# Performance work log

Hardware: AMD Instinct MI355X
Metric: run time of the kernel (lower is better)

The kernel has to match this reference:

```python
import jax, jax.numpy as jnp
import numpy as np

N = 100000
E = 3200000
D_IN = 128
D_OUT = 128


def setup_inputs() -> dict:
    key = jax.random.key(0)
    k1, k2, k3, k4, k5, k6, k7 = jax.random.split(key, 7)
    stdv = 1.0 / np.sqrt(D_OUT)
    x = jax.random.normal(k1, (N, D_IN), dtype=jnp.float32)
    rows = jax.random.randint(k2, (E,), 0, N, dtype=jnp.int32)
    cols = jax.random.randint(k3, (E,), 0, N, dtype=jnp.int32)
    edge_w = jax.random.uniform(k4, (E,), dtype=jnp.float32)
    W = jax.random.uniform(k5, (D_IN, D_OUT), minval=-stdv, maxval=stdv, dtype=jnp.float32)
    W_skip = jax.random.uniform(k6, (D_IN, D_OUT), minval=-stdv, maxval=stdv, dtype=jnp.float32)
    b = jax.random.uniform(k7, (D_OUT,), minval=-stdv, maxval=stdv, dtype=jnp.float32)
    return {"x": x, "rows": rows, "cols": cols, "edge_w": edge_w,
            "W": W, "W_skip": W_skip, "b": b}


def reference(x, rows, cols, edge_w, W, W_skip, b):
    # support1 = x @ W  [N, D_OUT]
    support1 = jnp.dot(x, W)
    # spmm(norm_adj, support1): out[r] = sum_{(r,c) in E} w_rc * support1[c]
    msgs = support1[cols] * edge_w[:, None]          # [E, D_OUT] gather
    agg = jax.ops.segment_sum(msgs, rows, num_segments=N)  # [N, D_OUT] scatter-add
    # skip connection + bias
    out = agg + jnp.dot(x, W_skip) + b
    return out
```

## Files before the change

kernel.cpp:

```cpp
#include <hip/hip_runtime.h>

#define D 128
#define B_LOG 7
#define ROWS_PB 128
#define MAX_NB 1024
#define GEMM_GRID 784
#define CHUNK_LOG 12

typedef short bf16x8 __attribute__((ext_vector_type(8)));
typedef float f32x4  __attribute__((ext_vector_type(4)));

static __device__ __forceinline__ unsigned short f2bf(float f) {
    unsigned u = __float_as_uint(f);
    u += 0x7FFFu + ((u >> 16) & 1u);
    return (unsigned short)(u >> 16);
}

__global__ __launch_bounds__(256) void wconv_kernel(
    const float* __restrict__ W, const float* __restrict__ Ws,
    short* __restrict__ Wt, int* __restrict__ bhist, int nb)
{
    const int idx = blockIdx.x * 256 + threadIdx.x;
    if (idx < 2 * D * D) {
        const int mat = idx >> 14;
        const int rem = idx & (D * D - 1);
        const int n = rem >> 7, k = rem & (D - 1);
        const float* src = mat ? Ws : W;
        Wt[idx] = (short)f2bf(src[k * D + n]);
    }
    if (idx < nb) bhist[idx] = 0;
}

__global__ __launch_bounds__(256) void bhist_kernel(
    const int* __restrict__ rows, int* __restrict__ bhist, int E, int nb)
{
    __shared__ int h[MAX_NB];
    const int t = threadIdx.x;
    for (int i = t; i < nb; i += 256) h[i] = 0;
    __syncthreads();

    int i = blockIdx.x * 256 + t;
    const int stride = gridDim.x * 256;
    for (; i < E; i += stride) atomicAdd(&h[rows[i] >> B_LOG], 1);
    __syncthreads();

    for (int i2 = t; i2 < nb; i2 += 256) {
        const int c = h[i2];
        if (c) atomicAdd(&bhist[i2], c);
    }
}

__global__ __launch_bounds__(256) void bscan_kernel(
    const int* __restrict__ bhist, int* __restrict__ bptr,
    int* __restrict__ bcur, int nb)
{
    const int t = threadIdx.x;
    const int base_i = t * 4;
    int v[4];
#pragma unroll
    for (int k = 0; k < 4; ++k)
        v[k] = (base_i + k < nb) ? bhist[base_i + k] : 0;
    const int s = v[0] + v[1] + v[2] + v[3];

    const int lane = t & 63, wv = t >> 6;
    int sc = s;
    for (int o = 1; o < 64; o <<= 1) {
        const int u = __shfl_up(sc, o, 64);
        if (lane >= o) sc += u;
    }
    __shared__ int wsum[4];
    if (lane == 63) wsum[wv] = sc;
    __syncthreads();

    int wbase = 0;
    for (int w2 = 0; w2 < wv; ++w2) wbase += wsum[w2];
    int excl = wbase + (sc - s);
#pragma unroll
    for (int k = 0; k < 4; ++k) {
        if (base_i + k < nb) { bptr[base_i + k] = excl; bcur[base_i + k] = excl; }
        excl += v[k];
    }
    if (t == 255) bptr[nb] = wsum[0] + wsum[1] + wsum[2] + wsum[3];
}

__global__ __launch_bounds__(256) void gemm_part_kernel(
    const float* __restrict__ x, const short* __restrict__ Wt,
    const float* __restrict__ b, unsigned short* __restrict__ s1b,
    unsigned short* __restrict__ skipb, int N,
    const int* __restrict__ rows, const int* __restrict__ cols,
    const float* __restrict__ ew, int* __restrict__ bcur,
    int2* __restrict__ se1, int E, int nb)
{
    __shared__ short sx[64 * D];

    const int t = threadIdx.x;

    if (blockIdx.x >= GEMM_GRID) {
        int* h = (int*)sx;
        const int nbl = gridDim.x - GEMM_GRID;
        const int nchunks = (E + (1 << CHUNK_LOG) - 1) >> CHUNK_LOG;

        for (int c = blockIdx.x - GEMM_GRID; c < nchunks; c += nbl) {
            const int ebeg = c << CHUNK_LOG;
            const int eend = min(ebeg + (1 << CHUNK_LOG), E);

            for (int i = t; i < nb; i += 256) h[i] = 0;
            __syncthreads();

            for (int e = ebeg + t; e < eend; e += 256)
                atomicAdd(&h[rows[e] >> B_LOG], 1);
            __syncthreads();

            for (int i = t; i < nb; i += 256) {
                const int cnt = h[i];
                h[i] = cnt ? atomicAdd(&bcur[i], cnt) : 0;
            }
            __syncthreads();

            for (int e = ebeg + t; e < eend; e += 256) {
                const int r    = rows[e];
                const int bkt  = r >> B_LOG;
                const int slot = atomicAdd(&h[bkt], 1);
                se1[slot] = make_int2(((r & (ROWS_PB - 1)) << 20) | cols[e],
                                      __float_as_int(ew[e]));
            }
            __syncthreads();
        }
        return;
    }

    const int lane = t & 63;
    const int w    = t >> 6;

    const int bmat = w >> 1;
    const int bn0  = (w & 1) * 64 + (lane & 15);
    const int bk0  = (lane >> 4) * 8;
    bf16x8 Bf[4][4];
#pragma unroll
    for (int nf = 0; nf < 4; ++nf)
#pragma unroll
        for (int ks = 0; ks < 4; ++ks)
            Bf[nf][ks] = *(const bf16x8*)&Wt[
                ((size_t)bmat * D + bn0 + nf * 16) * D + ks * 32 + bk0];

    float bias[4];
#pragma unroll
    for (int nf = 0; nf < 4; ++nf)
        bias[nf] = (w >= 2) ? b[(w - 2) * 64 + nf * 16 + (lane & 15)] : 0.f;

    const int ntiles = (N + 63) >> 6;
    const int trow = t >> 2;
    const int tk   = (t & 3) * 4;

    for (int rt = blockIdx.x; rt < ntiles; rt += GEMM_GRID) {
        const int r0 = rt << 6;
        __syncthreads();

        const int grow = min(r0 + trow, N - 1);
        const float* xrow = &x[(size_t)grow * D];
#pragma unroll
        for (int i = 0; i < 8; ++i) {
            const int k = tk + i * 16;
            const float4 v = *(const float4*)&xrow[k];
            const unsigned lo = (unsigned)f2bf(v.x) | ((unsigned)f2bf(v.y) << 16);
            const unsigned hi = (unsigned)f2bf(v.z) | ((unsigned)f2bf(v.w) << 16);
            unsigned byte = trow * 256 + k * 2;
            byte ^= (unsigned)((trow & 7) << 4);
            *(uint2*)((char*)sx + byte) = make_uint2(lo, hi);
        }
        __syncthreads();

        f32x4 acc[4][4];
#pragma unroll
        for (int mf = 0; mf < 4; ++mf)
#pragma unroll
            for (int nf = 0; nf < 4; ++nf)
                acc[mf][nf] = (f32x4){0.f, 0.f, 0.f, 0.f};

#pragma unroll
        for (int ks = 0; ks < 4; ++ks) {
            bf16x8 Af[4];
#pragma unroll
            for (int mf = 0; mf < 4; ++mf) {
                const int row = mf * 16 + (lane & 15);
                unsigned byte = row * 256 + (ks * 32 + bk0) * 2;
                byte ^= (unsigned)((row & 7) << 4);
                Af[mf] = *(const bf16x8*)((const char*)sx + byte);
            }
#pragma unroll
            for (int mf = 0; mf < 4; ++mf)
#pragma unroll
                for (int nf = 0; nf < 4; ++nf)
                    acc[mf][nf] = __builtin_amdgcn_mfma_f32_16x16x32_bf16(
                        Af[mf], Bf[nf][ks], acc[mf][nf], 0, 0, 0);
        }

#pragma unroll
        for (int mf = 0; mf < 4; ++mf) {
#pragma unroll
            for (int i = 0; i < 4; ++i) {
                const int row = r0 + mf * 16 + (lane >> 4) * 4 + i;
                if (row < N) {
                    if (w < 2) {
#pragma unroll
                        for (int nf = 0; nf < 4; ++nf) {
                            const int col = w * 64 + nf * 16 + (lane & 15);
                            s1b[(size_t)row * D + col] = f2bf(acc[mf][nf][i]);
                        }
                    } else {
#pragma unroll
                        for (int nf = 0; nf < 4; ++nf) {
                            const int col = (w - 2) * 64 + nf * 16 + (lane & 15);
                            skipb[(size_t)row * D + col] =
                                f2bf(acc[mf][nf][i] + bias[nf]);
                        }
                    }
                }
            }
        }
    }
}

__global__ __launch_bounds__(512) void binsort_kernel(
    const int* __restrict__ bptr, const int2* __restrict__ se1,
    int2* __restrict__ se2, int* __restrict__ rowptr, int N, int E)
{
    __shared__ int cnt[ROWS_PB];
    __shared__ int pos[ROWS_PB];
    const int t  = threadIdx.x;
    const int bk = blockIdx.x;
    const int r0 = bk << B_LOG;
    const int nr = min(ROWS_PB, N - r0);

    const int beg = bptr[bk];
    const int end = bptr[bk + 1];

    if (t < ROWS_PB) cnt[t] = 0;
    __syncthreads();

    for (int e = beg + t; e < end; e += 512)
        atomicAdd(&cnt[se1[e].x >> 20], 1);
    __syncthreads();

    if (t < ROWS_PB) pos[t] = cnt[t];
    __syncthreads();
#pragma unroll
    for (int off = 1; off < ROWS_PB; off <<= 1) {
        int v = (t < ROWS_PB && t >= off) ? pos[t - off] : 0;
        __syncthreads();
        if (t < ROWS_PB) pos[t] += v;
        __syncthreads();
    }
    if (t < ROWS_PB) {
        const int excl = beg + pos[t] - cnt[t];
        cnt[t] = excl;
        if (t < nr) rowptr[r0 + t] = excl;
    }
    if (t == 0 && r0 + nr == N) rowptr[N] = E;
    __syncthreads();

    for (int e = beg + t; e < end; e += 512) {
        const int2 rec = se1[e];
        const int  rl  = rec.x >> 20;
        const int  slot = atomicAdd(&cnt[rl], 1);
        se2[slot] = rec;
    }
}

__global__ __launch_bounds__(256) void spmm_csr_kernel(
    const unsigned short* __restrict__ s1b,
    const unsigned short* __restrict__ skipb,
    const int* __restrict__ rowptr, const int2* __restrict__ se,
    float* __restrict__ out, int N)
{
    const int lane = threadIdx.x & 63;
    const int wave = blockIdx.x * 4 + (threadIdx.x >> 6);
    const int nw   = gridDim.x * 4;
    const int j    = lane * 2;

    const long long* seq = (const long long*)se;

    for (int r = wave; r < N; r += nw) {
        const int beg = rowptr[r];
        const int end = rowptr[r + 1];

        float2 acc = make_float2(0.f, 0.f);
        int e = beg;
        for (; e + 8 <= end; e += 8) {
            long long ed[8];
#pragma unroll
            for (int k = 0; k < 8; ++k) ed[k] = seq[e + k];
            unsigned pk[8];
#pragma unroll
            for (int k = 0; k < 8; ++k)
                pk[k] = *(const unsigned*)&s1b[
                    (size_t)((unsigned)ed[k] & 0xFFFFFu) * D + j];
#pragma unroll
            for (int k = 0; k < 8; ++k) {
                const float w = __int_as_float((int)(ed[k] >> 32));
                acc.x = fmaf(w, __uint_as_float(pk[k] << 16), acc.x);
                acc.y = fmaf(w, __uint_as_float(pk[k] & 0xFFFF0000u), acc.y);
            }
        }
        for (; e < end; ++e) {
            const long long ed = seq[e];
            const unsigned pk = *(const unsigned*)&s1b[
                (size_t)((unsigned)ed & 0xFFFFFu) * D + j];
            const float w = __int_as_float((int)(ed >> 32));
            acc.x = fmaf(w, __uint_as_float(pk << 16), acc.x);
            acc.y = fmaf(w, __uint_as_float(pk & 0xFFFF0000u), acc.y);
        }

        const unsigned sk = *(const unsigned*)&skipb[(size_t)r * D + j];
        float2 o;
        o.x = acc.x + __uint_as_float(sk << 16);
        o.y = acc.y + __uint_as_float(sk & 0xFFFF0000u);
        *(float2*)&out[(size_t)r * D + j] = o;
    }
}

__global__ __launch_bounds__(512) void dual_gemm_fb_kernel(
    const float* __restrict__ x, const float* __restrict__ W,
    const float* __restrict__ Ws, const float* __restrict__ b,
    unsigned short* __restrict__ s1b, float* __restrict__ out, int N)
{
    __shared__ float sW[D * D];
    __shared__ float sWs[D * D];

    const int t = threadIdx.x;
    for (int i = t * 4; i < D * D; i += 512 * 4) {
        *(float4*)&sW[i]  = *(const float4*)&W[i];
        *(float4*)&sWs[i] = *(const float4*)&Ws[i];
    }
    __syncthreads();

    const int lane   = t & 63;
    const int wave   = blockIdx.x * 8 + (t >> 6);
    const int nwaves = gridDim.x * 8;
    const int j      = lane * 2;
    const float2 bb  = *(const float2*)&b[j];

    for (int r0 = wave * 4; r0 < N; r0 += nwaves * 4) {
        float2 xr[4];
#pragma unroll
        for (int r = 0; r < 4; ++r)
            xr[r] = *(const float2*)&x[(size_t)(r0 + r) * D + j];

        float2 a1[4], a2[4];
#pragma unroll
        for (int r = 0; r < 4; ++r) {
            a1[r] = make_float2(0.f, 0.f);
            a2[r] = make_float2(0.f, 0.f);
        }

#pragma unroll 8
        for (int k = 0; k < D; ++k) {
            const float2 wk  = *(const float2*)&sW[k * D + j];
            const float2 wsk = *(const float2*)&sWs[k * D + j];
#pragma unroll
            for (int r = 0; r < 4; ++r) {
                const float xv = __shfl((k & 1) ? xr[r].y : xr[r].x, k >> 1, 64);
                a1[r].x = fmaf(xv, wk.x,  a1[r].x);
                a1[r].y = fmaf(xv, wk.y,  a1[r].y);
                a2[r].x = fmaf(xv, wsk.x, a2[r].x);
                a2[r].y = fmaf(xv, wsk.y, a2[r].y);
            }
        }

#pragma unroll
        for (int r = 0; r < 4; ++r) {
            const unsigned pk = (unsigned)f2bf(a1[r].x) |
                                ((unsigned)f2bf(a1[r].y) << 16);
            *(unsigned*)&s1b[(size_t)(r0 + r) * D + j] = pk;
            *(float2*)&out[(size_t)(r0 + r) * D + j] =
                make_float2(a2[r].x + bb.x, a2[r].y + bb.y);
        }
    }
}

__global__ __launch_bounds__(256) void spmm_edges_kernel(
    const unsigned short* __restrict__ s1b, const int* __restrict__ rows,
    const int* __restrict__ cols, const float* __restrict__ ew,
    float* __restrict__ out, int E)
{
    const int lane = threadIdx.x & 63;
    const int wave = blockIdx.x * (blockDim.x >> 6) + (threadIdx.x >> 6);
    const int nw   = gridDim.x * (blockDim.x >> 6);
    const int j    = lane * 2;

    const int epw   = (E + nw - 1) / nw;
    const int e_beg = wave * epw;
    const int e_end = min(e_beg + epw, E);

    for (int e = e_beg; e < e_end; ++e) {
        const int   r = rows[e];
        const int   c = cols[e];
        const float w = ew[e];
        const unsigned p = *(const unsigned*)&s1b[(size_t)c * D + j];
        float* o = &out[(size_t)r * D + j];
        unsafeAtomicAdd(o,     w * __uint_as_float(p << 16));
        unsafeAtomicAdd(o + 1, w * __uint_as_float(p & 0xFFFF0000u));
    }
}

extern "C" void kernel_launch(void* const* d_in, const int* in_sizes, int n_in,
                              void* d_out, int out_size, void* d_ws, size_t ws_size,
                              hipStream_t stream) {
    const float* x    = (const float*)d_in[0];
    const int*   rows = (const int*)  d_in[1];
    const int*   cols = (const int*)  d_in[2];
    const float* ew   = (const float*)d_in[3];
    const float* W    = (const float*)d_in[4];
    const float* Ws   = (const float*)d_in[5];
    const float* b    = (const float*)d_in[6];
    float*       out  = (float*)d_out;

    const int N  = in_sizes[0] / D;
    const int E  = in_sizes[1];
    const int nb = (N + ROWS_PB - 1) >> B_LOG;

    const size_t s1_bytes   = ((size_t)N * D * 2 + 15) & ~(size_t)15;
    const size_t skip_bytes = s1_bytes;
    const size_t wt_bytes   = (size_t)2 * D * D * 2;
    const size_t int_bytes  = (((size_t)(3 * nb + N + 3)) * 4 + 7) & ~(size_t)7;
    const size_t need       = s1_bytes + skip_bytes + wt_bytes + int_bytes
                              + (size_t)E * 16;

    unsigned short* s1b = (unsigned short*)d_ws;

    if (ws_size >= need && nb <= MAX_NB) {
        unsigned short* skipb = (unsigned short*)((char*)d_ws + s1_bytes);
        short* Wt    = (short*)((char*)d_ws + s1_bytes + skip_bytes);
        int*   ibase = (int*)((char*)d_ws + s1_bytes + skip_bytes + wt_bytes);
        int*  bhist  = ibase;
        int*  bptr   = ibase + nb;
        int*  bcur   = ibase + 2 * nb + 1;
        int*  rowptr = ibase + 3 * nb + 1;
        int2* se1    = (int2*)((char*)d_ws + s1_bytes + skip_bytes + wt_bytes
                               + int_bytes);
        int2* se2    = se1 + E;

        wconv_kernel<<<(2 * D * D + 255) / 256, 256, 0, stream>>>(W, Ws, Wt, bhist, nb);
        bhist_kernel<<<512, 256, 0, stream>>>(rows, bhist, E, nb);
        bscan_kernel<<<1, 256, 0, stream>>>(bhist, bptr, bcur, nb);

        const int nchunks = (E + (1 << CHUNK_LOG) - 1) >> CHUNK_LOG;
        const int part_blocks = min(nchunks, 1024);
        gemm_part_kernel<<<GEMM_GRID + part_blocks, 256, 0, stream>>>(
            x, Wt, b, s1b, skipb, N, rows, cols, ew, bcur, se1, E, nb);

        binsort_kernel<<<nb, 512, 0, stream>>>(bptr, se1, se2, rowptr, N, E);
        spmm_csr_kernel<<<2048, 256, 0, stream>>>(s1b, skipb, rowptr, se2, out, N);
    } else {
        dual_gemm_fb_kernel<<<768, 512, 0, stream>>>(x, W, Ws, b, s1b, (float*)d_out, N);
        spmm_edges_kernel<<<2048, 256, 0, stream>>>(s1b, rows, cols, ew, (float*)d_out, E);
    }
}
```

Before: 243.5 us.

## Fuse bin-local row sort into SpMM using shared-memory edge buffer

Merges the per-bin counting sort and the CSR SpMM into one kernel. Each block sorts its bin's edges into LDS by local row, then each wave accumulates 16 rows straight from LDS. This removes the global se2 write and re-read, the rowptr array, and one launch. Bins larger than the LDS capacity fall back to global atomic adds. The trade-offs are heavy LDS use (36KB) per block, lower occupancy, and less load balancing, since nb is about 782 blocks of 512 threads.

```diff
diff --git a/kernel.cpp b/kernel.cpp
--- a/kernel.cpp
+++ b/kernel.cpp
@@ -6,6 +6,7 @@
 #define MAX_NB 1024
 #define GEMM_GRID 784
 #define CHUNK_LOG 12
+#define CAP 4608
 
 typedef short bf16x8 __attribute__((ext_vector_type(8)));
 typedef float f32x4  __attribute__((ext_vector_type(4)));
@@ -221,101 +222,122 @@
     }
 }
 
-__global__ __launch_bounds__(512) void binsort_kernel(
-    const int* __restrict__ bptr, const int2* __restrict__ se1,
-    int2* __restrict__ se2, int* __restrict__ rowptr, int N, int E)
-{
-    __shared__ int cnt[ROWS_PB];
-    __shared__ int pos[ROWS_PB];
-    const int t  = threadIdx.x;
-    const int bk = blockIdx.x;
-    const int r0 = bk << B_LOG;
-    const int nr = min(ROWS_PB, N - r0);
-
-    const int beg = bptr[bk];
-    const int end = bptr[bk + 1];
-
-    if (t < ROWS_PB) cnt[t] = 0;
-    __syncthreads();
-
-    for (int e = beg + t; e < end; e += 512)
-        atomicAdd(&cnt[se1[e].x >> 20], 1);
-    __syncthreads();
-
-    if (t < ROWS_PB) pos[t] = cnt[t];
-    __syncthreads();
-#pragma unroll
-    for (int off = 1; off < ROWS_PB; off <<= 1) {
-        int v = (t < ROWS_PB && t >= off) ? pos[t - off] : 0;
-        __syncthreads();
-        if (t < ROWS_PB) pos[t] += v;
-        __syncthreads();
-    }
-    if (t < ROWS_PB) {
-        const int excl = beg + pos[t] - cnt[t];
-        cnt[t] = excl;
-        if (t < nr) rowptr[r0 + t] = excl;
-    }
-    if (t == 0 && r0 + nr == N) rowptr[N] = E;
-    __syncthreads();
-
-    for (int e = beg + t; e < end; e += 512) {
-        const int2 rec = se1[e];
-        const int  rl  = rec.x >> 20;
-        const int  slot = atomicAdd(&cnt[rl], 1);
-        se2[slot] = rec;
-    }
-}
-
-__global__ __launch_bounds__(256) void spmm_csr_kernel(
+__global__ __launch_bounds__(512) void sortspmm_kernel(
     const unsigned short* __restrict__ s1b,
     const unsigned short* __restrict__ skipb,
-    const int* __restrict__ rowptr, const int2* __restrict__ se,
+    const int* __restrict__ bptr, const int2* __restrict__ se1,
     float* __restrict__ out, int N)
 {
-    const int lane = threadIdx.x & 63;
-    const int wave = blockIdx.x * 4 + (threadIdx.x >> 6);
-    const int nw   = gridDim.x * 4;
+    __shared__ long long recs[CAP];
+    __shared__ int rpos[ROWS_PB];
+    __shared__ int rcur[ROWS_PB];
+
+    const int t    = threadIdx.x;
+    const int lane = t & 63;
+    const int wv   = t >> 6;
+    const int bk   = blockIdx.x;
+    const int r0   = bk << B_LOG;
     const int j    = lane * 2;
 
-    const long long* seq = (const long long*)se;
-
-    for (int r = wave; r < N; r += nw) {
-        const int beg = rowptr[r];
-        const int end = rowptr[r + 1];
-
-        float2 acc = make_float2(0.f, 0.f);
-        int e = beg;
-        for (; e + 8 <= end; e += 8) {
-            long long ed[8];
-#pragma unroll
-            for (int k = 0; k < 8; ++k) ed[k] = seq[e + k];
-            unsigned pk[8];
-#pragma unroll
-            for (int k = 0; k < 8; ++k)
-                pk[k] = *(const unsigned*)&s1b[
-                    (size_t)((unsigned)ed[k] & 0xFFFFFu) * D + j];
-#pragma unroll
-            for (int k = 0; k < 8; ++k) {
-                const float w = __int_as_float((int)(ed[k] >> 32));
-                acc.x = fmaf(w, __uint_as_float(pk[k] << 16), acc.x);
-                acc.y = fmaf(w, __uint_as_float(pk[k] & 0xFFFF0000u), acc.y);
-            }
-        }
-        for (; e < end; ++e) {
+    const int beg  = bptr[bk];
+    const int end  = bptr[bk + 1];
+    const int cntE = end - beg;
+    const long long* seq = (const long long*)se1;
+
+    if (t < ROWS_PB) rcur[t] = 0;
+    __syncthreads();
+
+    for (int e = beg + t; e < end; e += 512)
+        atomicAdd(&rcur[(unsigned)se1[e].x >> 20], 1);
+    __syncthreads();
+
+    if (t < ROWS_PB) rpos[t] = rcur[t];
+    __syncthreads();
+#pragma unroll
+    for (int off = 1; off < ROWS_PB; off <<= 1) {
+        int v = (t < ROWS_PB && t >= off) ? rpos[t - off] : 0;
+        __syncthreads();
+        if (t < ROWS_PB) rpos[t] += v;
+        __syncthreads();
+    }
+    if (t < ROWS_PB) {
+        const int excl = rpos[t] - rcur[t];
+        rpos[t] = excl;
+        rcur[t] = excl;
+    }
+    __syncthreads();
+
+    if (cntE <= CAP) {
+        for (int e = beg + t; e < end; e += 512) {
+            const long long rec = seq[e];
+            const int rl = (int)((unsigned)rec >> 20);
+            const int slot = atomicAdd(&rcur[rl], 1);
+            recs[slot] = rec;
+        }
+        __syncthreads();
+
+        for (int i = 0; i < 16; ++i) {
+            const int rr = wv * 16 + i;
+            const int r  = r0 + rr;
+            if (r >= N) break;
+            int p        = rpos[rr];
+            const int pe = rcur[rr];
+
+            float2 acc = make_float2(0.f, 0.f);
+            for (; p + 8 <= pe; p += 8) {
+                long long ed[8];
+#pragma unroll
+                for (int k = 0; k < 8; ++k) ed[k] = recs[p + k];
+                unsigned pk[8];
+#pragma unroll
+                for (int k = 0; k < 8; ++k)
+                    pk[k] = *(const unsigned*)&s1b[
+                        (size_t)((unsigned)ed[k] & 0xFFFFFu) * D + j];
+#pragma unroll
+                for (int k = 0; k < 8; ++k) {
+                    const float w = __int_as_float((int)(ed[k] >> 32));
+                    acc.x = fmaf(w, __uint_as_float(pk[k] << 16), acc.x);
+                    acc.y = fmaf(w, __uint_as_float(pk[k] & 0xFFFF0000u), acc.y);
+                }
+            }
+            for (; p < pe; ++p) {
+                const long long ed = recs[p];
+                const unsigned pk = *(const unsigned*)&s1b[
+                    (size_t)((unsigned)ed & 0xFFFFFu) * D + j];
+                const float w = __int_as_float((int)(ed >> 32));
+                acc.x = fmaf(w, __uint_as_float(pk << 16), acc.x);
+                acc.y = fmaf(w, __uint_as_float(pk & 0xFFFF0000u), acc.y);
+            }
+
+            const unsigned sk = *(const unsigned*)&skipb[(size_t)r * D + j];
+            float2 o;
+            o.x = acc.x + __uint_as_float(sk << 16);
+            o.y = acc.y + __uint_as_float(sk & 0xFFFF0000u);
+            *(float2*)&out[(size_t)r * D + j] = o;
+        }
+    } else {
+        const int nr = min(ROWS_PB, N - r0);
+        for (int idx = t; idx < nr * 64; idx += 512) {
+            const int rr = idx >> 6;
+            const int cc = (idx & 63) * 2;
+            const unsigned sk = *(const unsigned*)&skipb[(size_t)(r0 + rr) * D + cc];
+            *(float2*)&out[(size_t)(r0 + rr) * D + cc] =
+                make_float2(__uint_as_float(sk << 16),
+                            __uint_as_float(sk & 0xFFFF0000u));
+        }
+        __syncthreads();
+
+        for (int e = beg + wv; e < end; e += 8) {
             const long long ed = seq[e];
+            const unsigned key = (unsigned)ed;
+            const int rl = (int)(key >> 20);
+            const float w = __int_as_float((int)(ed >> 32));
             const unsigned pk = *(const unsigned*)&s1b[
-                (size_t)((unsigned)ed & 0xFFFFFu) * D + j];
-            const float w = __int_as_float((int)(ed >> 32));
-            acc.x = fmaf(w, __uint_as_float(pk << 16), acc.x);
-            acc.y = fmaf(w, __uint_as_float(pk & 0xFFFF0000u), acc.y);
-        }
-
-        const unsigned sk = *(const unsigned*)&skipb[(size_t)r * D + j];
-        float2 o;
-        o.x = acc.x + __uint_as_float(sk << 16);
-        o.y = acc.y + __uint_as_float(sk & 0xFFFF0000u);
-        *(float2*)&out[(size_t)r * D + j] = o;
+                (size_t)(key & 0xFFFFFu) * D + j];
+            float* op = &out[(size_t)(r0 + rl) * D + j];
+            unsafeAtomicAdd(op,     w * __uint_as_float(pk << 16));
+            unsafeAtomicAdd(op + 1, w * __uint_as_float(pk & 0xFFFF0000u));
+        }
     }
 }
 
@@ -422,9 +444,9 @@
     const size_t s1_bytes   = ((size_t)N * D * 2 + 15) & ~(size_t)15;
     const size_t skip_bytes = s1_bytes;
     const size_t wt_bytes   = (size_t)2 * D * D * 2;
-    const size_t int_bytes  = (((size_t)(3 * nb + N + 3)) * 4 + 7) & ~(size_t)7;
+    const size_t int_bytes  = (((size_t)(3 * nb + 1)) * 4 + 7) & ~(size_t)7;
     const size_t need       = s1_bytes + skip_bytes + wt_bytes + int_bytes
-                              + (size_t)E * 16;
+                              + (size_t)E * 8;
 
     unsigned short* s1b = (unsigned short*)d_ws;
 
@@ -435,10 +457,8 @@
         int*  bhist  = ibase;
         int*  bptr   = ibase + nb;
         int*  bcur   = ibase + 2 * nb + 1;
-        int*  rowptr = ibase + 3 * nb + 1;
         int2* se1    = (int2*)((char*)d_ws + s1_bytes + skip_bytes + wt_bytes
                                + int_bytes);
-        int2* se2    = se1 + E;
 
         wconv_kernel<<<(2 * D * D + 255) / 256, 256, 0, stream>>>(W, Ws, Wt, bhist, nb);
         bhist_kernel<<<512, 256, 0, stream>>>(rows, bhist, E, nb);
@@ -449,8 +469,7 @@
         gemm_part_kernel<<<GEMM_GRID + part_blocks, 256, 0, stream>>>(
             x, Wt, b, s1b, skipb, N, rows, cols, ew, bcur, se1, E, nb);
 
-        binsort_kernel<<<nb, 512, 0, stream>>>(bptr, se1, se2, rowptr, N, E);
-        spmm_csr_kernel<<<2048, 256, 0, stream>>>(s1b, skipb, rowptr, se2, out, N);
+        sortspmm_kernel<<<nb, 512, 0, stream>>>(s1b, skipb, bptr, se1, out, N);
     } else {
         dual_gemm_fb_kernel<<<768, 512, 0, stream>>>(x, W, Ws, b, s1b, (float*)d_out, N);
         spmm_edges_kernel<<<2048, 256, 0, stream>>>(s1b, rows, cols, ew, (float*)d_out, E);
```

Result: faster. 221.0 us (-9.2%).
